# Kernel tuning notes

Measured on AMD Instinct MI355X. Metric: run time of the kernel, lower is better.

The kernel has to match this reference:

```python
import jax, jax.numpy as jnp
import numpy as np

BATCH, SEQ, D_MODEL, D_STATE = 8, 4096, 128, 128


def setup_inputs() -> dict:
    key = jax.random.key(0)
    ks = jax.random.split(key, 6)
    x = jax.random.normal(ks[0], (BATCH, SEQ, D_MODEL), jnp.float32)
    # Stable (negative) eigenvalues so A_discrete = exp(dt*Lambda) < 1 and powers don't overflow.
    Lam = -(jax.random.uniform(ks[1], (D_STATE,), jnp.float32) * 2.0 + 0.1)
    B = jax.random.normal(ks[2], (D_STATE, D_MODEL), jnp.float32) / np.sqrt(D_STATE)
    C = jax.random.normal(ks[3], (D_MODEL, D_STATE), jnp.float32) / np.sqrt(D_STATE)
    Dv = jax.random.normal(ks[4], (D_MODEL,), jnp.float32)
    log_dt = (jax.random.uniform(ks[5], (D_MODEL,), jnp.float32)
              * (np.log(0.001) - np.log(0.1)) + np.log(0.1)).astype(jnp.float32)
    return {"x": x, "Lam": Lam, "B": B, "C": C, "Dv": Dv, "log_dt": log_dt}


def _s4_forward(x, Lam, B, C, Dv, log_dt):
    # x: (batch, L, M) with transposed=False
    _, L, M = x.shape
    dt = jnp.exp(log_dt)                                    # (M,)
    rate = dt[:, None] * Lam[None, :]                       # (M, N) = log(A_discrete)
    ell = jnp.arange(L, dtype=x.dtype)                      # (L,)
    # powers[m, s, l] = A_discrete[m, s] ** l  (closed form of the sequential cumprod)
    powers = jnp.exp(rate[:, :, None] * ell[None, None, :])  # (M, N, L)
    # Original: einsum('ds,msl->dsl', B, powers) sums over m, giving B[d,s]*Psum[s,l];
    # then einsum('md,dsl->ml', C, .) contracts d and s -> kernel = C @ B @ Psum.
    Psum = powers.sum(axis=0)                               # (N, L)
    kernel = C @ (B @ Psum)                                 # (M, L)
    xt = jnp.transpose(x, (0, 2, 1))                        # (B, M, L)
    n = 2 * L  # zero-padded linear convolution via FFT
    y_fft = jnp.fft.rfft(xt, n=n) * jnp.fft.rfft(kernel, n=n)[None]
    y = jnp.fft.irfft(y_fft, n=n)[..., :L]                  # (B, M, L)
    y = y + Dv[None, :, None] * xt                          # skip connection D*u
    return jnp.transpose(y, (0, 2, 1))                      # (B, L, M)


def reference(x, Lam, B, C, Dv, log_dt):
    return _s4_forward(x, Lam, B, C, Dv, log_dt)
```

## Files before the change

kernel.cpp:

```cpp
#include <hip/hip_runtime.h>
#include <math.h>

#define BATCH 8
#define SEQ   4096
#define DM    128
#define DS    128
#define N2    4096
#define NT    256
#define NTP   256

__device__ __forceinline__ float2 cmulf(float2 a, float2 b) {
    return make_float2(a.x * b.x - a.y * b.y, a.x * b.y + a.y * b.x);
}
__device__ __forceinline__ float2 caddf(float2 a, float2 b) { return make_float2(a.x + b.x, a.y + b.y); }
__device__ __forceinline__ float2 csubf(float2 a, float2 b) { return make_float2(a.x - b.x, a.y - b.y); }
__device__ __forceinline__ float2 conjf2(float2 a) { return make_float2(a.x, -a.y); }
__device__ __forceinline__ float2 cisf(float t) { float s, c; __sincosf(t, &s, &c); return make_float2(c, s); }

__device__ __forceinline__ int nibrev(int k) { return ((k & 15) << 8) | (k & 0xF0) | (k >> 8); }
__device__ __forceinline__ int physi(int a) { return a ^ ((a >> 4) & 15); }
__device__ __forceinline__ int pqslot(int p) { return ((p & 15) << 8) | (p >> 4); }

__device__ __forceinline__ void dft16_fwd_l2(const float2 y[16], float2 Xh[16]) {
#pragma unroll
    for (int g = 0; g < 4; ++g) {
        float2 a0 = y[4*g], a1 = y[4*g+1], a2 = y[4*g+2], a3 = y[4*g+3];
        float2 t0 = caddf(a0,a2), t1 = csubf(a0,a2);
        float2 t2 = caddf(a1,a3), t3 = csubf(a1,a3);
        Xh[4*g]   = caddf(t0,t2);
        Xh[4*g+1] = make_float2(t1.x + t3.y, t1.y - t3.x);
        Xh[4*g+2] = csubf(t0,t2);
        Xh[4*g+3] = make_float2(t1.x - t3.y, t1.y + t3.x);
    }
}
__device__ __forceinline__ void dft16_inv_l2(const float2 y[16], float2 Xh[16]) {
#pragma unroll
    for (int g = 0; g < 4; ++g) {
        float2 a0 = y[4*g], a1 = y[4*g+1], a2 = y[4*g+2], a3 = y[4*g+3];
        float2 t0 = caddf(a0,a2), t1 = csubf(a0,a2);
        float2 t2 = caddf(a1,a3), t3 = csubf(a1,a3);
        Xh[4*g]   = caddf(t0,t2);
        Xh[4*g+1] = make_float2(t1.x - t3.y, t1.y + t3.x);
        Xh[4*g+2] = csubf(t0,t2);
        Xh[4*g+3] = make_float2(t1.x + t3.y, t1.y - t3.x);
    }
}

__device__ __forceinline__ void dft16_fwd(const float2 x[16], float2 Xh[16]) {
    const float2 W[10] = { {1.f,0.f},
        {0.92387953f,-0.38268343f},{0.70710678f,-0.70710678f},{0.38268343f,-0.92387953f},
        {0.f,-1.f},{-0.38268343f,-0.92387953f},{-0.70710678f,-0.70710678f},
        {-0.92387953f,-0.38268343f},{-1.f,0.f},{-0.92387953f,0.38268343f} };
    float2 y[16];
#pragma unroll
    for (int j = 0; j < 4; ++j) {
        float2 a0 = x[j], a1 = x[j+4], a2 = x[j+8], a3 = x[j+12];
        float2 t0 = caddf(a0,a2), t1 = csubf(a0,a2);
        float2 t2 = caddf(a1,a3), t3 = csubf(a1,a3);
        float2 b1 = make_float2(t1.x + t3.y, t1.y - t3.x);
        float2 b3 = make_float2(t1.x - t3.y, t1.y + t3.x);
        y[j]    = caddf(t0,t2);
        y[j+4]  = cmulf(b1, W[j]);
        y[j+8]  = cmulf(csubf(t0,t2), W[2*j]);
        y[j+12] = cmulf(b3, W[3*j]);
    }
    dft16_fwd_l2(y, Xh);
}

__device__ __forceinline__ void dft16_fwd_zh(const float2 x[8], float2 Xh[16]) {
    const float2 W[10] = { {1.f,0.f},
        {0.92387953f,-0.38268343f},{0.70710678f,-0.70710678f},{0.38268343f,-0.92387953f},
        {0.f,-1.f},{-0.38268343f,-0.92387953f},{-0.70710678f,-0.70710678f},
        {-0.92387953f,-0.38268343f},{-1.f,0.f},{-0.92387953f,0.38268343f} };
    float2 y[16];
#pragma unroll
    for (int j = 0; j < 4; ++j) {
        float2 a0 = x[j], a1 = x[j+4];
        float2 b1 = make_float2(a0.x + a1.y, a0.y - a1.x);
        float2 b3 = make_float2(a0.x - a1.y, a0.y + a1.x);
        y[j]    = caddf(a0, a1);
        y[j+4]  = cmulf(b1, W[j]);
        y[j+8]  = cmulf(csubf(a0, a1), W[2*j]);
        y[j+12] = cmulf(b3, W[3*j]);
    }
    dft16_fwd_l2(y, Xh);
}

__device__ __forceinline__ void dft16_inv(const float2 x[16], float2 Xh[16]) {
    const float2 W[10] = { {1.f,0.f},
        {0.92387953f,0.38268343f},{0.70710678f,0.70710678f},{0.38268343f,0.92387953f},
        {0.f,1.f},{-0.38268343f,0.92387953f},{-0.70710678f,0.70710678f},
        {-0.92387953f,0.38268343f},{-1.f,0.f},{-0.92387953f,-0.38268343f} };
    float2 y[16];
#pragma unroll
    for (int j = 0; j < 4; ++j) {
        float2 a0 = x[j], a1 = x[j+4], a2 = x[j+8], a3 = x[j+12];
        float2 t0 = caddf(a0,a2), t1 = csubf(a0,a2);
        float2 t2 = caddf(a1,a3), t3 = csubf(a1,a3);
        float2 b1 = make_float2(t1.x - t3.y, t1.y + t3.x);
        float2 b3 = make_float2(t1.x + t3.y, t1.y - t3.x);
        y[j]    = caddf(t0,t2);
        y[j+4]  = cmulf(b1, W[j]);
        y[j+8]  = cmulf(csubf(t0,t2), W[2*j]);
        y[j+12] = cmulf(b3, W[3*j]);
    }
    dft16_inv_l2(y, Xh);
}

__device__ __forceinline__ void dft16_inv_lo8(const float2 x[16], float2 out8[8]) {
    const float2 W[10] = { {1.f,0.f},
        {0.92387953f,0.38268343f},{0.70710678f,0.70710678f},{0.38268343f,0.92387953f},
        {0.f,1.f},{-0.38268343f,0.92387953f},{-0.70710678f,0.70710678f},
        {-0.92387953f,0.38268343f},{-1.f,0.f},{-0.92387953f,-0.38268343f} };
    float2 y[16];
#pragma unroll
    for (int j = 0; j < 4; ++j) {
        float2 a0 = x[j], a1 = x[j+4], a2 = x[j+8], a3 = x[j+12];
        float2 t0 = caddf(a0,a2), t1 = csubf(a0,a2);
        float2 t2 = caddf(a1,a3), t3 = csubf(a1,a3);
        float2 b1 = make_float2(t1.x - t3.y, t1.y + t3.x);
        float2 b3 = make_float2(t1.x + t3.y, t1.y - t3.x);
        y[j]    = caddf(t0,t2);
        y[j+4]  = cmulf(b1, W[j]);
        y[j+8]  = cmulf(csubf(t0,t2), W[2*j]);
        y[j+12] = cmulf(b3, W[3*j]);
    }
#pragma unroll
    for (int g = 0; g < 4; ++g) {
        float2 a0 = y[4*g], a1 = y[4*g+1], a2 = y[4*g+2], a3 = y[4*g+3];
        float2 t0 = caddf(a0,a2), t1 = csubf(a0,a2);
        float2 t2 = caddf(a1,a3), t3 = csubf(a1,a3);
        out8[g]   = caddf(t0,t2);
        out8[4+g] = make_float2(t1.x - t3.y, t1.y + t3.x);
    }
}

__device__ __forceinline__ void stage16_fwd(float2* z, int t) {
    float2 x[16], Xh[16];
    int adr[16];
    int j = t & 15, top = t >> 4;
#pragma unroll
    for (int r = 0; r < 16; ++r) adr[r] = (top << 8) + (r << 4) + (j ^ r);
#pragma unroll
    for (int r = 0; r < 16; ++r) x[r] = z[adr[r]];
    dft16_fwd(x, Xh);
    float ang = -(float)M_PI / 128.0f * (float)j;
    float2 w1 = cisf(ang);
    float2 wa = make_float2(1.f, 0.f);
    float2 wb = cisf(ang * 8.0f);
#pragma unroll
    for (int k = 0; k < 8; ++k) {
        int sk = ((k & 3) << 2) | (k >> 2);
        z[adr[k]]     = cmulf(Xh[sk],     wa);
        z[adr[k + 8]] = cmulf(Xh[sk + 2], wb);
        wa = cmulf(wa, w1);
        wb = cmulf(wb, w1);
    }
}

__device__ __forceinline__ void stage16_inv(float2* z, int t) {
    float2 x[16], Xh[16];
    int adr[16];
    int j = t & 15, top = t >> 4;
#pragma unroll
    for (int r = 0; r < 16; ++r) adr[r] = (top << 8) + (r << 4) + (j ^ r);
    float ang = (float)M_PI / 128.0f * (float)j;
    float2 w1 = cisf(ang);
    float2 wa = make_float2(1.f, 0.f);
    float2 wb = cisf(ang * 8.0f);
#pragma unroll
    for (int k = 0; k < 8; ++k) {
        x[k]     = cmulf(z[adr[k]],     wa);
        x[k + 8] = cmulf(z[adr[k + 8]], wb);
        wa = cmulf(wa, w1);
        wb = cmulf(wb, w1);
    }
    dft16_inv(x, Xh);
#pragma unroll
    for (int r = 0; r < 16; ++r) {
        int sr = ((r & 3) << 2) | (r >> 2);
        z[adr[r]] = Xh[sr];
    }
}

__device__ __forceinline__ void stage1_fwd_keep(float2* z, int t, float2 v[16]) {
    float2 x[16], Xh[16];
    int adr[16];
    int j4 = t & 15;
#pragma unroll
    for (int r = 0; r < 16; ++r) adr[r] = (t << 4) + (j4 ^ r);
#pragma unroll
    for (int r = 0; r < 16; ++r) x[r] = z[adr[r]];
    dft16_fwd(x, Xh);
#pragma unroll
    for (int k = 0; k < 16; ++k) {
        int sk = ((k & 3) << 2) | (k >> 2);
        v[k] = Xh[sk];
        z[adr[k]] = v[k];
    }
}

__device__ __forceinline__ void fwd_first(float2* z, const float2* __restrict__ vrow, int t) {
    float2 x8[8], Xh[16];
#pragma unroll
    for (int r = 0; r < 8; ++r) x8[r] = vrow[t + (r << 8)];
    dft16_fwd_zh(x8, Xh);
    int b0 = t ^ ((t >> 4) & 15);
    float ang = -(float)M_PI / 2048.0f * (float)t;
    float2 w1 = cisf(ang);
    float2 wa = make_float2(1.f, 0.f);
    float2 wb = cisf(ang * 8.0f);
#pragma unroll
    for (int k = 0; k < 8; ++k) {
        int sk = ((k & 3) << 2) | (k >> 2);
        z[b0 + (k << 8)]       = cmulf(Xh[sk],     wa);
        z[b0 + ((k + 8) << 8)] = cmulf(Xh[sk + 2], wb);
        wa = cmulf(wa, w1);
        wb = cmulf(wb, w1);
    }
}

__device__ __forceinline__ void inv_last_store(const float2* z, float2* __restrict__ xrow,
                                               int t, float dv) {
    float2 x[16], out8[8];
    int b0 = t ^ ((t >> 4) & 15);
    float ang = (float)M_PI / 2048.0f * (float)t;
    float2 w1 = cisf(ang);
    float2 wa = make_float2(1.f, 0.f);
    float2 wb = cisf(ang * 8.0f);
#pragma unroll
    for (int k = 0; k < 8; ++k) {
        x[k]     = cmulf(z[b0 + (k << 8)],       wa);
        x[k + 8] = cmulf(z[b0 + ((k + 8) << 8)], wb);
        wa = cmulf(wa, w1);
        wb = cmulf(wb, w1);
    }
    dft16_inv_lo8(x, out8);
    const float invN = 1.0f / 4096.0f;
#pragma unroll
    for (int r = 0; r < 8; ++r) {
        float2 res = out8[r];
        float2 xv = xrow[t + (r << 8)];
        xrow[t + (r << 8)] = make_float2(res.x * invN + dv * xv.x, res.y * invN + dv * xv.y);
    }
}

__device__ __forceinline__ void pq_one_e(float2 Kk, float2 Kkp, float2 e,
                                         float2 fap, float2 fbp,
                                         float2* P, float2* Q) {
    float2 fa = make_float2(0.5f * (1.f + e.y), -0.5f * e.x);
    float2 fb = make_float2(0.5f * (1.f - e.y),  0.5f * e.x);
    float2 ak = cmulf(Kk, fa), bk = cmulf(Kk, fb);
    float2 apv = cmulf(Kkp, fap), bpv = cmulf(Kkp, fbp);
    float2 g = make_float2(0.5f * (1.f + e.y), 0.5f * e.x);
    float2 h = make_float2(0.5f * (1.f - e.y), -0.5f * e.x);
    *P = caddf(cmulf(g, ak), cmulf(h, conjf2(bpv)));
    *Q = caddf(cmulf(g, bk), cmulf(h, conjf2(apv)));
}
__device__ __forceinline__ void pq_pair_e(float2 Kk, float2 Kkp, float2 e,
                                          float2* Pk, float2* Qk, float2* Pkp, float2* Qkp) {
    float2 ep = make_float2(-e.x, e.y);
    float2 fa  = make_float2(0.5f * (1.f + e.y),  -0.5f * e.x);
    float2 fb  = make_float2(0.5f * (1.f - e.y),   0.5f * e.x);
    float2 fap = make_float2(0.5f * (1.f + ep.y), -0.5f * ep.x);
    float2 fbp = make_float2(0.5f * (1.f - ep.y),  0.5f * ep.x);
    pq_one_e(Kk,  Kkp, e,  fap, fbp, Pk,  Qk);
    pq_one_e(Kkp, Kk,  ep, fa,  fb,  Pkp, Qkp);
}

__global__ void __launch_bounds__(NTP) prep_fused(
    const float* __restrict__ Lam, const float* __restrict__ logdt, float* __restrict__ Psum,
    const float* __restrict__ Cm, const float* __restrict__ Bm, float* __restrict__ GT,
    const float* __restrict__ x, float* __restrict__ xt) {
    __shared__ float E[DM];
    __shared__ float tile[32][33];
    int bid = blockIdx.x, t = threadIdx.x;
    if (bid < 256) {
        int s = bid >> 1, half = bid & 1;
        if (t < DM) E[t] = __expf(logdt[t]) * Lam[s];
        __syncthreads();
        int l0 = t + 2048 * half;
        float acc[8] = {0.f,0.f,0.f,0.f,0.f,0.f,0.f,0.f};
        for (int m = 0; m < DM; ++m) {
            float e = E[m];
            float w = __expf(e * (float)l0);
            float r = __expf(e * 256.0f);
#pragma unroll
            for (int i = 0; i < 8; ++i) { acc[i] += w; w *= r; }
        }
#pragma unroll
        for (int i = 0; i < 8; ++i) Psum[s * SEQ + l0 + 256 * i] = acc[i];
    } else if (bid < 320) {
        int gid = (bid - 256) * NTP + t;
        int m = gid >> 7, j = gid & 127;
        float acc = 0.f;
        for (int i = 0; i < DS; ++i) acc += Cm[m * DS + i] * Bm[i * DM + j];
        GT[j * DM + m] = acc;
    } else {
        int u = bid - 320;
        int b = u >> 9;
        int m0 = ((u >> 7) & 3) * 32;
        int l0 = (u & 127) * 32;
        int lr = t >> 3, mc4 = (t & 7) * 4;
        float4 v = *(const float4*)&x[(size_t)b * SEQ * DM + (size_t)(l0 + lr) * DM + m0 + mc4];
        tile[lr][mc4 + 0] = v.x; tile[lr][mc4 + 1] = v.y;
        tile[lr][mc4 + 2] = v.z; tile[lr][mc4 + 3] = v.w;
        __syncthreads();
        int mr = t >> 3, lc4 = (t & 7) * 4;
        float4 o = make_float4(tile[lc4 + 0][mr], tile[lc4 + 1][mr],
                               tile[lc4 + 2][mr], tile[lc4 + 3][mr]);
        *(float4*)&xt[(size_t)b * DM * SEQ + (size_t)(m0 + mr) * SEQ + l0 + lc4] = o;
    }
}

__global__ void prep_K2(const float* __restrict__ GT, const float* __restrict__ Psum,
                        float* __restrict__ K) {
    __shared__ float4 PT[DS][4];
    int l0 = blockIdx.x * 16;
    int t = threadIdx.x;
    for (int idx = t; idx < 512; idx += NTP) {
        int s = idx >> 2, q = idx & 3;
        PT[s][q] = ((const float4*)(Psum + s * SEQ + l0))[q];
    }
    __syncthreads();
    int m = t & 127, half = t >> 7;
    float acc[8] = {0.f,0.f,0.f,0.f,0.f,0.f,0.f,0.f};
    for (int s = 0; s < DS; ++s) {
        float g = GT[s * DM + m];
        float4 p0 = PT[s][half * 2], p1 = PT[s][half * 2 + 1];
        acc[0] += g * p0.x; acc[1] += g * p0.y; acc[2] += g * p0.z; acc[3] += g * p0.w;
        acc[4] += g * p1.x; acc[5] += g * p1.y; acc[6] += g * p1.z; acc[7] += g * p1.w;
    }
    float4* kp = (float4*)(K + (size_t)m * SEQ + l0 + half * 8);
    kp[0] = make_float4(acc[0], acc[1], acc[2], acc[3]);
    kp[1] = make_float4(acc[4], acc[5], acc[6], acc[7]);
}

template<int C0>
__device__ __forceinline__ void pq_epilogue(const float2 v[16], const float2* z,
                                            float4* __restrict__ dst, int t) {
#pragma unroll
    for (int cc = 0; cc < 4; ++cc) {
        const int c = C0 + cc;
        int pos = (t << 4) | c;
        float2 Pk, Qk, Pkp, Qkp;
        if (pos == 0) {
            float2 v0 = v[0];
            float2 v2 = v[8];
            float2 Ku0    = make_float2(v0.x + v0.y, 0.f);
            float2 Ku4096 = make_float2(v0.x - v0.y, 0.f);
            float2 Ku2048 = conjf2(v2);
            float2 Pd, Qd;
            pq_pair_e(Ku0, Ku4096, make_float2(1.f, 0.f), &Pk, &Qk, &Pd, &Qd);
            float2 Pd2, Qd2;
            pq_pair_e(Ku2048, Ku2048, make_float2(0.f, -1.f), &Pkp, &Qkp, &Pd2, &Qd2);
            dst[pqslot(0)] = make_float4(Pk.x, Pk.y, Qk.x, Qk.y);
            dst[pqslot(8)] = make_float4(Pkp.x, Pkp.y, Qkp.x, Qkp.y);
        } else {
            int k  = nibrev(pos);
            int kp = 4096 - k;
            int ppos = nibrev(kp);
            float2 va = v[c];
            float2 vb = z[physi(ppos)];
            float thk = (float)M_PI * (float)k / 4096.0f;
            float2 e  = cisf(-thk);
            float2 cb = conjf2(vb);
            float2 s  = caddf(va, cb), d = csubf(va, cb);
            float2 pr = cmulf(e, d);
            float2 Kuk = make_float2(0.5f * (s.x + pr.y), 0.5f * (s.y - pr.x));
            float2 ep = make_float2(-e.x, e.y);
            float2 ca = conjf2(va);
            float2 s2 = caddf(vb, ca), d2 = csubf(vb, ca);
            float2 p2 = cmulf(ep, d2);
            float2 Kukp = make_float2(0.5f * (s2.x + p2.y), 0.5f * (s2.y - p2.x));
            pq_pair_e(Kuk, Kukp, e, &Pk, &Qk, &Pkp, &Qkp);
            dst[pqslot(pos)]  = make_float4(Pk.x, Pk.y, Qk.x, Qk.y);
            dst[pqslot(ppos)] = make_float4(Pkp.x, Pkp.y, Qkp.x, Qkp.y);
        }
    }
}

__global__ void __launch_bounds__(NT, 4) fftK_PQ(const float* __restrict__ K,
                                                 float4* __restrict__ PQ) {
    __shared__ __align__(16) float2 z[N2];
    int t = threadIdx.x;
    int m = blockIdx.x & (DM - 1);
    int half = blockIdx.x >> 7;
    const float2* krow = (const float2*)(K + (size_t)m * SEQ);

    fwd_first(z, krow, t);  __syncthreads();
    stage16_fwd(z, t);      __syncthreads();
    float2 v[16];
    stage1_fwd_keep(z, t, v); __syncthreads();

    float4* dst = PQ + (size_t)m * 4096;
    if (half == 0) pq_epilogue<0>(v, z, dst, t);
    else           pq_epilogue<4>(v, z, dst, t);
}

__global__ void __launch_bounds__(NT, 4) conv16(float* __restrict__ xt,
                                                const float4* __restrict__ PQ,
                                                const float* __restrict__ Dv) {
    __shared__ __align__(16) float2 z[N2];
    int t = threadIdx.x;
    int m = blockIdx.x & (DM - 1);
    int b = blockIdx.x >> 7;
    float2* xrow = (float2*)(xt + (((size_t)b * DM + m) << 12));

    fwd_first(z, xrow, t);  __syncthreads();
    stage16_fwd(z, t);      __syncthreads();
    float2 v[16];
    stage1_fwd_keep(z, t, v); __syncthreads();

    {
        const float4* pq = PQ + (size_t)m * 4096;
#pragma unroll
        for (int r = 0; r < 16; ++r) {
            int pos = (t << 4) | r;
            int k  = nibrev(pos);
            int kp = (4096 - k) & 4095;
            float2 vb = z[physi(nibrev(kp))];
            float4 co = pq[(r << 8) | t];
            v[r] = caddf(cmulf(make_float2(co.x, co.y), v[r]),
                         cmulf(make_float2(co.z, co.w), conjf2(vb)));
        }
    }
    __syncthreads();
    {
        float2 Xh[16];
        dft16_inv(v, Xh);
        int j4 = t & 15;
#pragma unroll
        for (int r = 0; r < 16; ++r) {
            int sr = ((r & 3) << 2) | (r >> 2);
            z[(t << 4) + (r ^ j4)] = Xh[sr];
        }
    }
    __syncthreads();

    stage16_inv(z, t);      __syncthreads();
    inv_last_store(z, xrow, t, Dv[m]);
}

__global__ void transpose_yout(const float* __restrict__ yt, float* __restrict__ out) {
    __shared__ float tile[32][33];
    int b = blockIdx.z;
    int l0 = blockIdx.x * 32, m0 = blockIdx.y * 32;
    int t = threadIdx.x;
    int mr = t >> 3, lc4 = (t & 7) * 4;
    float4 v = *(const float4*)&yt[(size_t)b * DM * SEQ + (size_t)(m0 + mr) * SEQ + l0 + lc4];
    tile[mr][lc4 + 0] = v.x; tile[mr][lc4 + 1] = v.y;
    tile[mr][lc4 + 2] = v.z; tile[mr][lc4 + 3] = v.w;
    __syncthreads();
    int lr = t >> 3, mc4 = (t & 7) * 4;
    float4 o = make_float4(tile[mc4 + 0][lr], tile[mc4 + 1][lr],
                           tile[mc4 + 2][lr], tile[mc4 + 3][lr]);
    *(float4*)&out[(size_t)b * SEQ * DM + (size_t)(l0 + lr) * DM + m0 + mc4] = o;
}

extern "C" void kernel_launch(void* const* d_in, const int* in_sizes, int n_in,
                              void* d_out, int out_size, void* d_ws, size_t ws_size,
                              hipStream_t stream) {
    const float* x     = (const float*)d_in[0];
    const float* Lam   = (const float*)d_in[1];
    const float* Bm    = (const float*)d_in[2];
    const float* Cm    = (const float*)d_in[3];
    const float* Dv    = (const float*)d_in[4];
    const float* logdt = (const float*)d_in[5];
    float* out = (float*)d_out;

    float*  ws   = (float*)d_ws;
    float*  xt   = ws;
    float4* PQ   = (float4*)(ws + 4194304);
    float*  K    = ws + 4194304 + 2097152;
    float*  Psum = K + 524288;
    float*  GT   = Psum + 524288;

    hipLaunchKernelGGL(prep_fused,     dim3(4416),       dim3(NTP),  0, stream,
                       Lam, logdt, Psum, Cm, Bm, GT, x, xt);
    hipLaunchKernelGGL(prep_K2,        dim3(256),        dim3(NTP),  0, stream, GT, Psum, K);
    hipLaunchKernelGGL(fftK_PQ,        dim3(256),        dim3(NT),   0, stream, K, PQ);
    hipLaunchKernelGGL(conv16,         dim3(1024),       dim3(NT),   0, stream, xt, PQ, Dv);
    hipLaunchKernelGGL(transpose_yout, dim3(128, 4, 8),  dim3(NT),   0, stream, xt, out);
}
```

Measured before the change: 124.5 us.

## Fuse input and output transposes into the FFT convolution kernel

After: 138.3 us. +11.1%, slower.

```diff
diff --git a/kernel.cpp b/kernel.cpp
--- a/kernel.cpp
+++ b/kernel.cpp
@@ -200,10 +200,8 @@
     }
 }
 
-__device__ __forceinline__ void fwd_first(float2* z, const float2* __restrict__ vrow, int t) {
-    float2 x8[8], Xh[16];
-#pragma unroll
-    for (int r = 0; r < 8; ++r) x8[r] = vrow[t + (r << 8)];
+__device__ __forceinline__ void fwd_first_reg(float2* z, const float2 x8[8], int t) {
+    float2 Xh[16];
     dft16_fwd_zh(x8, Xh);
     int b0 = t ^ ((t >> 4) & 15);
     float ang = -(float)M_PI / 2048.0f * (float)t;
@@ -220,8 +218,15 @@
     }
 }
 
-__device__ __forceinline__ void inv_last_store(const float2* z, float2* __restrict__ xrow,
-                                               int t, float dv) {
+__device__ __forceinline__ void fwd_first(float2* z, const float2* __restrict__ vrow, int t) {
+    float2 x8[8];
+#pragma unroll
+    for (int r = 0; r < 8; ++r) x8[r] = vrow[t + (r << 8)];
+    fwd_first_reg(z, x8, t);
+}
+
+__device__ __forceinline__ void inv_last_store_direct(const float2* z, float* __restrict__ orow,
+                                                      int t, float dv, const float2 x8[8]) {
     float2 x[16], out8[8];
     int b0 = t ^ ((t >> 4) & 15);
     float ang = (float)M_PI / 2048.0f * (float)t;
@@ -240,8 +245,9 @@
 #pragma unroll
     for (int r = 0; r < 8; ++r) {
         float2 res = out8[r];
-        float2 xv = xrow[t + (r << 8)];
-        xrow[t + (r << 8)] = make_float2(res.x * invN + dv * xv.x, res.y * invN + dv * xv.y);
+        int l = (t + (r << 8)) << 1;
+        orow[(size_t)l * DM]       = res.x * invN + dv * x8[r].x;
+        orow[(size_t)(l + 1) * DM] = res.y * invN + dv * x8[r].y;
     }
 }
 
@@ -266,74 +272,6 @@
     float2 fbp = make_float2(0.5f * (1.f - ep.y),  0.5f * ep.x);
     pq_one_e(Kk,  Kkp, e,  fap, fbp, Pk,  Qk);
     pq_one_e(Kkp, Kk,  ep, fa,  fb,  Pkp, Qkp);
-}
-
-__global__ void __launch_bounds__(NTP) prep_fused(
-    const float* __restrict__ Lam, const float* __restrict__ logdt, float* __restrict__ Psum,
-    const float* __restrict__ Cm, const float* __restrict__ Bm, float* __restrict__ GT,
-    const float* __restrict__ x, float* __restrict__ xt) {
-    __shared__ float E[DM];
-    __shared__ float tile[32][33];
-    int bid = blockIdx.x, t = threadIdx.x;
-    if (bid < 256) {
-        int s = bid >> 1, half = bid & 1;
-        if (t < DM) E[t] = __expf(logdt[t]) * Lam[s];
-        __syncthreads();
-        int l0 = t + 2048 * half;
-        float acc[8] = {0.f,0.f,0.f,0.f,0.f,0.f,0.f,0.f};
-        for (int m = 0; m < DM; ++m) {
-            float e = E[m];
-            float w = __expf(e * (float)l0);
-            float r = __expf(e * 256.0f);
-#pragma unroll
-            for (int i = 0; i < 8; ++i) { acc[i] += w; w *= r; }
-        }
-#pragma unroll
-        for (int i = 0; i < 8; ++i) Psum[s * SEQ + l0 + 256 * i] = acc[i];
-    } else if (bid < 320) {
-        int gid = (bid - 256) * NTP + t;
-        int m = gid >> 7, j = gid & 127;
-        float acc = 0.f;
-        for (int i = 0; i < DS; ++i) acc += Cm[m * DS + i] * Bm[i * DM + j];
-        GT[j * DM + m] = acc;
-    } else {
-        int u = bid - 320;
-        int b = u >> 9;
-        int m0 = ((u >> 7) & 3) * 32;
-        int l0 = (u & 127) * 32;
-        int lr = t >> 3, mc4 = (t & 7) * 4;
-        float4 v = *(const float4*)&x[(size_t)b * SEQ * DM + (size_t)(l0 + lr) * DM + m0 + mc4];
-        tile[lr][mc4 + 0] = v.x; tile[lr][mc4 + 1] = v.y;
-        tile[lr][mc4 + 2] = v.z; tile[lr][mc4 + 3] = v.w;
-        __syncthreads();
-        int mr = t >> 3, lc4 = (t & 7) * 4;
-        float4 o = make_float4(tile[lc4 + 0][mr], tile[lc4 + 1][mr],
-                               tile[lc4 + 2][mr], tile[lc4 + 3][mr]);
-        *(float4*)&xt[(size_t)b * DM * SEQ + (size_t)(m0 + mr) * SEQ + l0 + lc4] = o;
-    }
-}
-
-__global__ void prep_K2(const float* __restrict__ GT, const float* __restrict__ Psum,
-                        float* __restrict__ K) {
-    __shared__ float4 PT[DS][4];
-    int l0 = blockIdx.x * 16;
-    int t = threadIdx.x;
-    for (int idx = t; idx < 512; idx += NTP) {
-        int s = idx >> 2, q = idx & 3;
-        PT[s][q] = ((const float4*)(Psum + s * SEQ + l0))[q];
-    }
-    __syncthreads();
-    int m = t & 127, half = t >> 7;
-    float acc[8] = {0.f,0.f,0.f,0.f,0.f,0.f,0.f,0.f};
-    for (int s = 0; s < DS; ++s) {
-        float g = GT[s * DM + m];
-        float4 p0 = PT[s][half * 2], p1 = PT[s][half * 2 + 1];
-        acc[0] += g * p0.x; acc[1] += g * p0.y; acc[2] += g * p0.z; acc[3] += g * p0.w;
-        acc[4] += g * p1.x; acc[5] += g * p1.y; acc[6] += g * p1.z; acc[7] += g * p1.w;
-    }
-    float4* kp = (float4*)(K + (size_t)m * SEQ + l0 + half * 8);
-    kp[0] = make_float4(acc[0], acc[1], acc[2], acc[3]);
-    kp[1] = make_float4(acc[4], acc[5], acc[6], acc[7]);
 }
 
 template<int C0>
@@ -380,6 +318,58 @@
     }
 }
 
+__global__ void __launch_bounds__(NTP) prep_GP(
+    const float* __restrict__ Lam, const float* __restrict__ logdt, float* __restrict__ Psum,
+    const float* __restrict__ Cm, const float* __restrict__ Bm, float* __restrict__ GT) {
+    __shared__ float E[DM];
+    int bid = blockIdx.x, t = threadIdx.x;
+    if (bid < 256) {
+        int s = bid >> 1, half = bid & 1;
+        if (t < DM) E[t] = __expf(logdt[t]) * Lam[s];
+        __syncthreads();
+        int l0 = t + 2048 * half;
+        float acc[8] = {0.f,0.f,0.f,0.f,0.f,0.f,0.f,0.f};
+        for (int m = 0; m < DM; ++m) {
+            float e = E[m];
+            float w = __expf(e * (float)l0);
+            float r = __expf(e * 256.0f);
+#pragma unroll
+            for (int i = 0; i < 8; ++i) { acc[i] += w; w *= r; }
+        }
+#pragma unroll
+        for (int i = 0; i < 8; ++i) Psum[s * SEQ + l0 + 256 * i] = acc[i];
+    } else {
+        int gid = (bid - 256) * NTP + t;
+        int m = gid >> 7, j = gid & 127;
+        float acc = 0.f;
+        for (int i = 0; i < DS; ++i) acc += Cm[m * DS + i] * Bm[i * DM + j];
+        GT[j * DM + m] = acc;
+    }
+}
+
+__global__ void prep_K2(const float* __restrict__ GT, const float* __restrict__ Psum,
+                        float* __restrict__ K) {
+    __shared__ float4 PT[DS][4];
+    int l0 = blockIdx.x * 16;
+    int t = threadIdx.x;
+    for (int idx = t; idx < 512; idx += NTP) {
+        int s = idx >> 2, q = idx & 3;
+        PT[s][q] = ((const float4*)(Psum + s * SEQ + l0))[q];
+    }
+    __syncthreads();
+    int m = t & 127, half = t >> 7;
+    float acc[8] = {0.f,0.f,0.f,0.f,0.f,0.f,0.f,0.f};
+    for (int s = 0; s < DS; ++s) {
+        float g = GT[s * DM + m];
+        float4 p0 = PT[s][half * 2], p1 = PT[s][half * 2 + 1];
+        acc[0] += g * p0.x; acc[1] += g * p0.y; acc[2] += g * p0.z; acc[3] += g * p0.w;
+        acc[4] += g * p1.x; acc[5] += g * p1.y; acc[6] += g * p1.z; acc[7] += g * p1.w;
+    }
+    float4* kp = (float4*)(K + (size_t)m * SEQ + l0 + half * 8);
+    kp[0] = make_float4(acc[0], acc[1], acc[2], acc[3]);
+    kp[1] = make_float4(acc[4], acc[5], acc[6], acc[7]);
+}
+
 __global__ void __launch_bounds__(NT, 4) fftK_PQ(const float* __restrict__ K,
                                                  float4* __restrict__ PQ) {
     __shared__ __align__(16) float2 z[N2];
@@ -398,17 +388,28 @@
     else           pq_epilogue<4>(v, z, dst, t);
 }
 
-__global__ void __launch_bounds__(NT, 4) conv16(float* __restrict__ xt,
-                                                const float4* __restrict__ PQ,
-                                                const float* __restrict__ Dv) {
+__global__ void __launch_bounds__(NT, 4) conv_direct(const float* __restrict__ x,
+                                                     float* __restrict__ out,
+                                                     const float4* __restrict__ PQ,
+                                                     const float* __restrict__ Dv) {
     __shared__ __align__(16) float2 z[N2];
     int t = threadIdx.x;
-    int m = blockIdx.x & (DM - 1);
-    int b = blockIdx.x >> 7;
-    float2* xrow = (float2*)(xt + (((size_t)b * DM + m) << 12));
-
-    fwd_first(z, xrow, t);  __syncthreads();
-    stage16_fwd(z, t);      __syncthreads();
+    int bid = blockIdx.x;
+    int m = ((bid & 7) << 4) | ((bid >> 3) & 15);
+    int b = bid >> 7;
+    const float* xrow = x   + (size_t)b * SEQ * DM + m;
+    float*       orow = out + (size_t)b * SEQ * DM + m;
+
+    float2 x8[8];
+#pragma unroll
+    for (int r = 0; r < 8; ++r) {
+        int l = (t + (r << 8)) << 1;
+        x8[r].x = xrow[(size_t)l * DM];
+        x8[r].y = xrow[(size_t)(l + 1) * DM];
+    }
+
+    fwd_first_reg(z, x8, t); __syncthreads();
+    stage16_fwd(z, t);       __syncthreads();
     float2 v[16];
     stage1_fwd_keep(z, t, v); __syncthreads();
 
@@ -439,23 +440,7 @@
     __syncthreads();
 
     stage16_inv(z, t);      __syncthreads();
-    inv_last_store(z, xrow, t, Dv[m]);
-}
-
-__global__ void transpose_yout(const float* __restrict__ yt, float* __restrict__ out) {
-    __shared__ float tile[32][33];
-    int b = blockIdx.z;
-    int l0 = blockIdx.x * 32, m0 = blockIdx.y * 32;
-    int t = threadIdx.x;
-    int mr = t >> 3, lc4 = (t & 7) * 4;
-    float4 v = *(const float4*)&yt[(size_t)b * DM * SEQ + (size_t)(m0 + mr) * SEQ + l0 + lc4];
-    tile[mr][lc4 + 0] = v.x; tile[mr][lc4 + 1] = v.y;
-    tile[mr][lc4 + 2] = v.z; tile[mr][lc4 + 3] = v.w;
-    __syncthreads();
-    int lr = t >> 3, mc4 = (t & 7) * 4;
-    float4 o = make_float4(tile[mc4 + 0][lr], tile[mc4 + 1][lr],
-                           tile[mc4 + 2][lr], tile[mc4 + 3][lr]);
-    *(float4*)&out[(size_t)b * SEQ * DM + (size_t)(l0 + lr) * DM + m0 + mc4] = o;
+    inv_last_store_direct(z, orow, t, Dv[m], x8);
 }
 
 extern "C" void kernel_launch(void* const* d_in, const int* in_sizes, int n_in,
@@ -470,16 +455,13 @@
     float* out = (float*)d_out;
 
     float*  ws   = (float*)d_ws;
-    float*  xt   = ws;
-    float4* PQ   = (float4*)(ws + 4194304);
-    float*  K    = ws + 4194304 + 2097152;
+    float4* PQ   = (float4*)ws;
+    float*  K    = ws + 2097152;
     float*  Psum = K + 524288;
     float*  GT   = Psum + 524288;
 
-    hipLaunchKernelGGL(prep_fused,     dim3(4416),       dim3(NTP),  0, stream,
-                       Lam, logdt, Psum, Cm, Bm, GT, x, xt);
-    hipLaunchKernelGGL(prep_K2,        dim3(256),        dim3(NTP),  0, stream, GT, Psum, K);
-    hipLaunchKernelGGL(fftK_PQ,        dim3(256),        dim3(NT),   0, stream, K, PQ);
-    hipLaunchKernelGGL(conv16,         dim3(1024),       dim3(NT),   0, stream, xt, PQ, Dv);
-    hipLaunchKernelGGL(transpose_yout, dim3(128, 4, 8),  dim3(NT),   0, stream, xt, out);
-}
+    hipLaunchKernelGGL(prep_GP,     dim3(320),  dim3(NTP), 0, stream, Lam, logdt, Psum, Cm, Bm, GT);
+    hipLaunchKernelGGL(prep_K2,     dim3(256),  dim3(NTP), 0, stream, GT, Psum, K);
+    hipLaunchKernelGGL(fftK_PQ,     dim3(256),  dim3(NT),  0, stream, K, PQ);
+    hipLaunchKernelGGL(conv_direct, dim3(1024), dim3(NT),  0, stream, x, out, PQ, Dv);
+}
```
